# Optimization experiments

Hardware: AMD Instinct MI355X
Metric: run time of the kernel (lower is better)

## Reference

```python
import jax, jax.numpy as jnp
import numpy as np
from jax import lax

B, C, H, W = 4, 64, 96, 96
K = 9  # 3x3 kernel taps


def setup_inputs() -> dict:
    key = jax.random.key(0)
    k1, k2, k3 = jax.random.split(key, 3)
    x = jax.random.normal(k1, (B, C, H, W), dtype=jnp.float32)
    # offset conv: small init so predicted offsets are modest (deform conv convention)
    w_off = jax.random.normal(k2, (18, C, 3, 3), dtype=jnp.float32) * 0.01
    b_off = jnp.zeros((18,), dtype=jnp.float32)
    # main deformable conv weights (fan-in scaled)
    w_dc = jax.random.normal(k3, (C, C, 3, 3), dtype=jnp.float32) * (1.0 / np.sqrt(C * 9))
    b_dc = jnp.zeros((C,), dtype=jnp.float32)
    return {"x": x, "w_off": w_off, "b_off": b_off, "w_dc": w_dc, "b_dc": b_dc}


def _deform_conv(x, offset, w_dc, b_dc):
    # x: [B,C,H,W]; offset: [B,2K,H,W] laid out as (dy,dx) per tap, row-major taps
    b, c, h, w = x.shape
    off = offset.reshape(b, K, 2, h, w)
    ky, kx = jnp.meshgrid(jnp.arange(3), jnp.arange(3), indexing="ij")
    ky = ky.reshape(K).astype(x.dtype)  # tap row offsets 0..2
    kx = kx.reshape(K).astype(x.dtype)
    hh = jnp.arange(h, dtype=x.dtype)[None, None, :, None]
    ww = jnp.arange(w, dtype=x.dtype)[None, None, None, :]
    pad = 1.0
    # absolute sampling coordinates [B,K,H,W]
    py = hh + (ky - pad)[None, :, None, None] + off[:, :, 0]
    px = ww + (kx - pad)[None, :, None, None] + off[:, :, 1]

    y0 = jnp.floor(py)
    x0 = jnp.floor(px)
    ly = (py - y0)[:, None]  # [B,1,K,H,W]
    lx = (px - x0)[:, None]
    y0i = y0.astype(jnp.int32)
    x0i = x0.astype(jnp.int32)

    x_flat = x.reshape(b, c, h * w)

    def gather(yi, xi):
        valid = (yi >= 0) & (yi < h) & (xi >= 0) & (xi < w)
        yc = jnp.clip(yi, 0, h - 1)
        xc = jnp.clip(xi, 0, w - 1)
        idx = (yc * w + xc).reshape(b, 1, K * h * w)
        v = jnp.take_along_axis(x_flat, idx, axis=2).reshape(b, c, K, h, w)
        return v * valid.astype(x.dtype)[:, None]  # zero padding outside image

    v00 = gather(y0i, x0i)
    v01 = gather(y0i, x0i + 1)
    v10 = gather(y0i + 1, x0i)
    v11 = gather(y0i + 1, x0i + 1)
    samp = (v00 * (1 - ly) * (1 - lx) + v01 * (1 - ly) * lx
            + v10 * ly * (1 - lx) + v11 * ly * lx)  # [B,C,K,H,W]

    out = jnp.einsum("bckhw,ock->bohw", samp, w_dc.reshape(c, c, K))
    return out + b_dc[None, :, None, None]


def reference(x, w_off, b_off, w_dc, b_dc):
    offset = lax.conv_general_dilated(
        x, w_off, window_strides=(1, 1), padding=((1, 1), (1, 1)),
        dimension_numbers=("NCHW", "OIHW", "NCHW"))
    offset = offset + b_off[None, :, None, None]
    return _deform_conv(x, offset, w_dc, b_dc)
```

## Files before the change

kernel.cpp:

```cpp
#include <hip/hip_runtime.h>
#include <math.h>

typedef _Float16 h4    __attribute__((ext_vector_type(4)));
typedef _Float16 half8 __attribute__((ext_vector_type(8)));
typedef float    f32x4 __attribute__((ext_vector_type(4)));

constexpr int B = 4, C = 64, H = 96, W = 96;
constexpr int NQ = C / 4;
constexpr int KT = 9, OFFC = 18;
constexpr int HW = H * W;
constexpr int PAD = 4;
constexpr int HP = H + 2 * PAD, WP = W + 2 * PAD;
constexpr int HPWP = HP * WP;
constexpr int WDF_HALFS = 4 * KT * 2 * 64 * 8;
constexpr int WOF_HALFS = 2 * KT * 2 * 64 * 8;

struct h4x2 { h4 a, b; };

__global__ __launch_bounds__(256) void prep(
        const float* __restrict__ x, const float* __restrict__ w_off,
        const float* __restrict__ w_dc,
        h4* __restrict__ xpad4, _Float16* __restrict__ wdf,
        _Float16* __restrict__ wof) {
    const int i = blockIdx.x * 256 + threadIdx.x;
    {
        int col = i % WP; int t = i / WP; int row = t % HP; int bq = t / HP;
        int b = bq / NQ, q = bq % NQ;
        int h = row - PAD, w = col - PAD;
        h4 v; v[0] = v[1] = v[2] = v[3] = (_Float16)0.f;
        if (h >= 0 && h < H && w >= 0 && w < W) {
            const float* xp = x + ((size_t)b * C + 4 * q) * HW + h * W + w;
            v[0] = (_Float16)xp[0];
            v[1] = (_Float16)xp[HW];
            v[2] = (_Float16)xp[2 * HW];
            v[3] = (_Float16)xp[3 * HW];
        }
        xpad4[i] = v;
    }
    if (i < WDF_HALFS) {
        int m = i / 9216, r = i % 9216;
        int tap = r / 1024, l = (r >> 3) & 63, j = i & 7;
        int ks = (r >> 9) & 1;
        int o = m * 16 + (l & 15);
        int c = ks * 32 + ((l >> 4) << 3) + j;
        wdf[i] = (_Float16)w_dc[((size_t)o * C + c) * KT + tap];
    }
    if (i < WOF_HALFS) {
        int mf = i / 9216, r = i % 9216;
        int tap = r / 1024, l = (r >> 3) & 63, j = i & 7;
        int ks = (r >> 9) & 1;
        int oc = mf * 16 + (l & 15);
        int c = ks * 32 + ((l >> 4) << 3) + j;
        wof[i] = (oc < OFFC) ? (_Float16)w_off[((size_t)oc * C + c) * KT + tap]
                             : (_Float16)0.f;
    }
}

__global__ __launch_bounds__(256, 2) void fused_wave(
        const h4* __restrict__ xpad4, const _Float16* __restrict__ wdf,
        const _Float16* __restrict__ wof, const float* __restrict__ b_off,
        const float* __restrict__ b_dc, float* __restrict__ out) {
    const int lane = threadIdx.x & 63;
    const int wid = __builtin_amdgcn_readfirstlane(threadIdx.x >> 6);
    const int p = lane & 15, g = lane >> 4;
    const int bid = blockIdx.x;
    const int tile = (bid & 7) * 72 + (bid >> 3);
    const int wt = tile * 4 + wid;
    const int flat0 = wt * 16;
    const int b_u = __builtin_amdgcn_readfirstlane(flat0 / HW);
    const int loc0 = flat0 - b_u * HW;
    const int h = loc0 / W;
    const int w = loc0 % W + p;

    __shared__ _Float16 wlds[WDF_HALFS];
    __shared__ float offt[4][2 * KT][16];

    {
        #pragma unroll
        for (int s2 = 0; s2 < 18; ++s2) {
            const int seg = wid * 18 + s2;
            __builtin_amdgcn_global_load_lds(
                (const __attribute__((address_space(1))) unsigned int*)
                    (wdf + (size_t)seg * 512 + lane * 8),
                (__attribute__((address_space(3))) unsigned int*)
                    &wlds[seg * 512],
                16, 0, 0);
        }
    }

    const h4* xq = xpad4 + (size_t)b_u * NQ * HPWP;

    {
        f32x4 a0 = {0.f,0.f,0.f,0.f}, a1 = {0.f,0.f,0.f,0.f};
        half8 bf[2][2];
        half8 wcA[4], wnA[4];
        const _Float16* wofb = wof + lane * 8;

        auto loadWA = [&](half8* dst, int k) {
            #pragma unroll
            for (int ks = 0; ks < 2; ++ks) {
                dst[2 * ks]     = *(const half8*)(wofb + k * 1024 + ks * 512);
                dst[2 * ks + 1] = *(const half8*)(wofb + 9216 + k * 1024 + ks * 512);
            }
        };
        auto issueA = [&](int s, int k) {
            const int cell = (h + k / 3 - 1 + PAD) * WP + (w + k % 3 - 1 + PAD);
            #pragma unroll
            for (int ks = 0; ks < 2; ++ks) {
                h4 q0 = xq[(size_t)(ks * 8 + 2 * g)     * HPWP + cell];
                h4 q1 = xq[(size_t)(ks * 8 + 2 * g + 1) * HPWP + cell];
                bf[s][ks] = __builtin_shufflevector(q0, q1, 0,1,2,3,4,5,6,7);
            }
        };
        auto mfmaA = [&](int s, const half8* wa) {
            #pragma unroll
            for (int ks = 0; ks < 2; ++ks) {
                a0 = __builtin_amdgcn_mfma_f32_16x16x32_f16(wa[2*ks],   bf[s][ks], a0, 0, 0, 0);
                a1 = __builtin_amdgcn_mfma_f32_16x16x32_f16(wa[2*ks+1], bf[s][ks], a1, 0, 0, 0);
            }
        };

        loadWA(wcA, 0);
        issueA(0, 0); issueA(1, 1);
        #pragma unroll
        for (int k = 1; k <= 8; ++k) {
            loadWA(wnA, k);
            __builtin_amdgcn_sched_barrier(0);
            mfmaA((k - 1) & 1, wcA);
            __builtin_amdgcn_sched_barrier(0);
            if (k < 8) issueA((k - 1) & 1, k + 1);
            #pragma unroll
            for (int q2 = 0; q2 < 4; ++q2) wcA[q2] = wnA[q2];
        }
        mfmaA(0, wcA);

        #pragma unroll
        for (int r = 0; r < 4; ++r) {
            const int oc = g * 4 + r;
            offt[wid][oc][p] = a0[r] + b_off[oc];
        }
        if (g == 0) {
            #pragma unroll
            for (int r = 0; r < 2; ++r)
                offt[wid][16 + r][p] = a1[r] + b_off[16 + r];
        }
    }
    __syncthreads();

    {
        f32x4 acc[4] = {{0.f,0.f,0.f,0.f},{0.f,0.f,0.f,0.f},
                        {0.f,0.f,0.f,0.f},{0.f,0.f,0.f,0.f}};
        h4x2 rt[2][2][2], rb[2][2][2];
        h4 Wc[2][4];
        const _Float16* wl = wlds + lane * 8;

        auto issueB = [&](int s, int k) {
            const float dy = offt[wid][2 * k][p];
            const float dx = offt[wid][2 * k + 1][p];
            const float py = (float)(h + k / 3 - 1) + dy;
            const float px = (float)(w + k % 3 - 1) + dx;
            const float y0f = floorf(py), x0f = floorf(px);
            const float ly = py - y0f, lx = px - x0f;
            int y0 = (int)y0f, x0 = (int)x0f;
            y0 = min(max(y0, -PAD), H + PAD - 2);
            x0 = min(max(x0, -PAD), W + PAD - 2);
            const int base = (y0 + PAD) * WP + (x0 + PAD);
            const float a11 = ly * lx;
            const _Float16 f11 = (_Float16)a11;
            const _Float16 f10 = (_Float16)(ly - a11);
            const _Float16 f01 = (_Float16)(lx - a11);
            const _Float16 f00 = (_Float16)(1.f - ly - lx + a11);
            #pragma unroll
            for (int e = 0; e < 4; ++e) { Wc[s][0][e] = f00; Wc[s][1][e] = f01;
                                          Wc[s][2][e] = f10; Wc[s][3][e] = f11; }
            #pragma unroll
            for (int ks = 0; ks < 2; ++ks) {
                #pragma unroll
                for (int q2 = 0; q2 < 2; ++q2) {
                    const h4* qp = xq + (size_t)(ks * 8 + 2 * g + q2) * HPWP + base;
                    __builtin_memcpy(&rt[s][ks][q2], qp, 16);
                    __builtin_memcpy(&rb[s][ks][q2], qp + WP, 16);
                }
            }
        };
        auto mfmaB = [&](int s, int k) {
            #pragma unroll
            for (int ks = 0; ks < 2; ++ks) {
                h4 s0 = rt[s][ks][0].a * Wc[s][0] + rt[s][ks][0].b * Wc[s][1]
                      + rb[s][ks][0].a * Wc[s][2] + rb[s][ks][0].b * Wc[s][3];
                h4 s1 = rt[s][ks][1].a * Wc[s][0] + rt[s][ks][1].b * Wc[s][1]
                      + rb[s][ks][1].a * Wc[s][2] + rb[s][ks][1].b * Wc[s][3];
                half8 bfr = __builtin_shufflevector(s0, s1, 0,1,2,3,4,5,6,7);
                #pragma unroll
                for (int m = 0; m < 4; ++m) {
                    half8 wf = *(const half8*)(wl + m * 9216 + k * 1024 + ks * 512);
                    acc[m] = __builtin_amdgcn_mfma_f32_16x16x32_f16(wf, bfr,
                                                                    acc[m], 0, 0, 0);
                }
            }
        };

        issueB(0, 0); issueB(1, 1);
        #pragma unroll
        for (int k = 1; k <= 8; ++k) {
            __builtin_amdgcn_sched_barrier(0);
            mfmaB((k - 1) & 1, k - 1);
            __builtin_amdgcn_sched_barrier(0);
            if (k < 8) issueB((k - 1) & 1, k + 1);
        }
        mfmaB(0, 8);

        #pragma unroll
        for (int m = 0; m < 4; ++m) {
            #pragma unroll
            for (int r = 0; r < 4; ++r) {
                const int o = m * 16 + g * 4 + r;
                out[((size_t)b_u * C + o) * HW + loc0 + p] = acc[m][r] + b_dc[o];
            }
        }
    }
}

extern "C" void kernel_launch(void* const* d_in, const int* in_sizes, int n_in,
                              void* d_out, int out_size, void* d_ws, size_t ws_size,
                              hipStream_t stream) {
    const float* x     = (const float*)d_in[0];
    const float* w_off = (const float*)d_in[1];
    const float* b_off = (const float*)d_in[2];
    const float* w_dc  = (const float*)d_in[3];
    const float* b_dc  = (const float*)d_in[4];
    float* out = (float*)d_out;

    char* ws = (char*)d_ws;
    h4*        xpad4 = (h4*)ws;
    _Float16*  wdf   = (_Float16*)(ws + 5537792);
    _Float16*  wof   = (_Float16*)(ws + 5537792 + 73728);

    prep<<<B * NQ * HPWP / 256, 256, 0, stream>>>(x, w_off, w_dc, xpad4, wdf, wof);
    fused_wave<<<576, 256, 0, stream>>>(xpad4, wdf, wof, b_off, b_dc, out);
}
```

Before: 30.40 us.

## Deepen load pipelines to three stages, add MFMA priority, defer weight LDS copy

Both the offset-conv and deformable-conv phases now prefetch three taps ahead instead of two, using triple-buffered registers. The offset-conv weights are double-buffered by slot index rather than copied each iteration. The async global-to-LDS copy of the main conv weights now starts after the offset MFMAs are issued, so the gathers for phase A are not queued behind it. s_setprio raises wave priority around the MFMA bursts. The deeper buffering adds register pressure, which could lower occupancy or cause spills.

```diff
diff --git a/kernel.cpp b/kernel.cpp
--- a/kernel.cpp
+++ b/kernel.cpp
@@ -75,7 +75,51 @@
     __shared__ _Float16 wlds[WDF_HALFS];
     __shared__ float offt[4][2 * KT][16];
 
+    const h4* xq = xpad4 + (size_t)b_u * NQ * HPWP;
+
     {
+        f32x4 a0 = {0.f,0.f,0.f,0.f}, a1 = {0.f,0.f,0.f,0.f};
+        half8 bf[3][2];
+        half8 wA[2][4];
+        const _Float16* wofb = wof + lane * 8;
+
+        auto loadWA = [&](int slot, int k) {
+            #pragma unroll
+            for (int ks = 0; ks < 2; ++ks) {
+                wA[slot][2 * ks]     = *(const half8*)(wofb + k * 1024 + ks * 512);
+                wA[slot][2 * ks + 1] = *(const half8*)(wofb + 9216 + k * 1024 + ks * 512);
+            }
+        };
+        auto issueA = [&](int s, int k) {
+            const int cell = (h + k / 3 - 1 + PAD) * WP + (w + k % 3 - 1 + PAD);
+            #pragma unroll
+            for (int ks = 0; ks < 2; ++ks) {
+                h4 q0 = xq[(size_t)(ks * 8 + 2 * g)     * HPWP + cell];
+                h4 q1 = xq[(size_t)(ks * 8 + 2 * g + 1) * HPWP + cell];
+                bf[s][ks] = __builtin_shufflevector(q0, q1, 0,1,2,3,4,5,6,7);
+            }
+        };
+        auto mfmaA = [&](int s, int slot) {
+            __builtin_amdgcn_s_setprio(1);
+            #pragma unroll
+            for (int ks = 0; ks < 2; ++ks) {
+                a0 = __builtin_amdgcn_mfma_f32_16x16x32_f16(wA[slot][2*ks],   bf[s][ks], a0, 0, 0, 0);
+                a1 = __builtin_amdgcn_mfma_f32_16x16x32_f16(wA[slot][2*ks+1], bf[s][ks], a1, 0, 0, 0);
+            }
+            __builtin_amdgcn_s_setprio(0);
+        };
+
+        loadWA(0, 0); loadWA(1, 1);
+        issueA(0, 0); issueA(1, 1); issueA(2, 2);
+        #pragma unroll
+        for (int k = 1; k <= 8; ++k) {
+            __builtin_amdgcn_sched_barrier(0);
+            mfmaA((k - 1) % 3, (k - 1) & 1);
+            __builtin_amdgcn_sched_barrier(0);
+            if (k <= 7) loadWA((k - 1) & 1, k + 1);
+            if (k <= 6) issueA((k - 1) % 3, k + 2);
+        }
+
         #pragma unroll
         for (int s2 = 0; s2 < 18; ++s2) {
             const int seg = wid * 18 + s2;
@@ -86,53 +130,8 @@
                     &wlds[seg * 512],
                 16, 0, 0);
         }
-    }
-
-    const h4* xq = xpad4 + (size_t)b_u * NQ * HPWP;
-
-    {
-        f32x4 a0 = {0.f,0.f,0.f,0.f}, a1 = {0.f,0.f,0.f,0.f};
-        half8 bf[2][2];
-        half8 wcA[4], wnA[4];
-        const _Float16* wofb = wof + lane * 8;
-
-        auto loadWA = [&](half8* dst, int k) {
-            #pragma unroll
-            for (int ks = 0; ks < 2; ++ks) {
-                dst[2 * ks]     = *(const half8*)(wofb + k * 1024 + ks * 512);
-                dst[2 * ks + 1] = *(const half8*)(wofb + 9216 + k * 1024 + ks * 512);
-            }
-        };
-        auto issueA = [&](int s, int k) {
-            const int cell = (h + k / 3 - 1 + PAD) * WP + (w + k % 3 - 1 + PAD);
-            #pragma unroll
-            for (int ks = 0; ks < 2; ++ks) {
-                h4 q0 = xq[(size_t)(ks * 8 + 2 * g)     * HPWP + cell];
-                h4 q1 = xq[(size_t)(ks * 8 + 2 * g + 1) * HPWP + cell];
-                bf[s][ks] = __builtin_shufflevector(q0, q1, 0,1,2,3,4,5,6,7);
-            }
-        };
-        auto mfmaA = [&](int s, const half8* wa) {
-            #pragma unroll
-            for (int ks = 0; ks < 2; ++ks) {
-                a0 = __builtin_amdgcn_mfma_f32_16x16x32_f16(wa[2*ks],   bf[s][ks], a0, 0, 0, 0);
-                a1 = __builtin_amdgcn_mfma_f32_16x16x32_f16(wa[2*ks+1], bf[s][ks], a1, 0, 0, 0);
-            }
-        };
-
-        loadWA(wcA, 0);
-        issueA(0, 0); issueA(1, 1);
-        #pragma unroll
-        for (int k = 1; k <= 8; ++k) {
-            loadWA(wnA, k);
-            __builtin_amdgcn_sched_barrier(0);
-            mfmaA((k - 1) & 1, wcA);
-            __builtin_amdgcn_sched_barrier(0);
-            if (k < 8) issueA((k - 1) & 1, k + 1);
-            #pragma unroll
-            for (int q2 = 0; q2 < 4; ++q2) wcA[q2] = wnA[q2];
-        }
-        mfmaA(0, wcA);
+        __builtin_amdgcn_sched_barrier(0);
+        mfmaA(8 % 3, 8 & 1);
 
         #pragma unroll
         for (int r = 0; r < 4; ++r) {
@@ -150,8 +149,8 @@
     {
         f32x4 acc[4] = {{0.f,0.f,0.f,0.f},{0.f,0.f,0.f,0.f},
                         {0.f,0.f,0.f,0.f},{0.f,0.f,0.f,0.f}};
-        h4x2 rt[2][2][2], rb[2][2][2];
-        h4 Wc[2][4];
+        h4x2 rt[3][2][2], rb[3][2][2];
+        h4 Wc[3][4];
         const _Float16* wl = wlds + lane * 8;
 
         auto issueB = [&](int s, int k) {
@@ -191,24 +190,26 @@
                 h4 s1 = rt[s][ks][1].a * Wc[s][0] + rt[s][ks][1].b * Wc[s][1]
                       + rb[s][ks][1].a * Wc[s][2] + rb[s][ks][1].b * Wc[s][3];
                 half8 bfr = __builtin_shufflevector(s0, s1, 0,1,2,3,4,5,6,7);
+                __builtin_amdgcn_s_setprio(1);
                 #pragma unroll
                 for (int m = 0; m < 4; ++m) {
                     half8 wf = *(const half8*)(wl + m * 9216 + k * 1024 + ks * 512);
                     acc[m] = __builtin_amdgcn_mfma_f32_16x16x32_f16(wf, bfr,
                                                                     acc[m], 0, 0, 0);
                 }
-            }
-        };
-
-        issueB(0, 0); issueB(1, 1);
+                __builtin_amdgcn_s_setprio(0);
+            }
+        };
+
+        issueB(0, 0); issueB(1, 1); issueB(2, 2);
         #pragma unroll
         for (int k = 1; k <= 8; ++k) {
             __builtin_amdgcn_sched_barrier(0);
-            mfmaB((k - 1) & 1, k - 1);
-            __builtin_amdgcn_sched_barrier(0);
-            if (k < 8) issueB((k - 1) & 1, k + 1);
-        }
-        mfmaB(0, 8);
+            mfmaB((k - 1) % 3, k - 1);
+            __builtin_amdgcn_sched_barrier(0);
+            if (k <= 6) issueB((k - 1) % 3, k + 2);
+        }
+        mfmaB(8 % 3, 8);
 
         #pragma unroll
         for (int m = 0; m < 4; ++m) {
```

After: 30.87 us. Within noise of the previous version (+1.6%).
